# Performance work log

Measured on AMD Instinct MI355X. Metric: run time of the kernel, lower is better.

The kernel has to match this reference:

```python
import jax, jax.numpy as jnp
import numpy as np
import math

B, S, E, H, FF = 8, 1024, 1024, 16, 4096
HD = E // H
N_DOM = 1024          # boolean-domain size used in the custom scale
LN_EPS = 1e-5


def _layernorm(x, g, b, eps=LN_EPS):
    mu = jnp.mean(x, axis=-1, keepdims=True)
    var = jnp.var(x, axis=-1, keepdims=True)
    return (x - mu) * jax.lax.rsqrt(var + eps) * g + b


def setup_inputs() -> dict:
    key = jax.random.key(0)
    ks = jax.random.split(key, 8)
    s_e = 1.0 / math.sqrt(E)
    s_f = 1.0 / math.sqrt(FF)
    return {
        "x": jax.random.normal(ks[0], (B, S, E), jnp.float32),
        "in_proj_w": jax.random.normal(ks[1], (3 * E, E), jnp.float32) * s_e,
        "out_proj_w": jax.random.normal(ks[2], (E, E), jnp.float32) * s_e,
        "ln1_g": jnp.ones((E,), jnp.float32),
        "ln1_b": jnp.zeros((E,), jnp.float32),
        "ln2_g": jnp.ones((E,), jnp.float32),
        "ln2_b": jnp.zeros((E,), jnp.float32),
        "w1": jax.random.normal(ks[3], (FF, E), jnp.float32) * s_e,
        "b1": jax.random.normal(ks[4], (FF,), jnp.float32) * 0.01,
        "w2": jax.random.normal(ks[5], (E, FF), jnp.float32) * s_f,
        "b2": jax.random.normal(ks[6], (E,), jnp.float32) * 0.01,
    }


def reference(x, in_proj_w, out_proj_w, ln1_g, ln1_b, ln2_g, ln2_b, w1, b1, w2, b2):
    # --- custom multi-head attention (bias=False, dropout=0) ---
    qkv = jnp.einsum("bse,fe->bsf", x, in_proj_w)              # [B,S,3E]
    q, k, v = jnp.split(qkv, 3, axis=-1)
    q = q.reshape(B, S, H, HD)
    k = k.reshape(B, S, H, HD)
    v = v.reshape(B, S, H, HD)
    # nonstandard scale: sqrt(1/head_dim) * 2 * log(N)
    scale = math.sqrt(1.0 / HD) * 2.0 * math.log(N_DOM)
    scores = jnp.einsum("bqhd,bkhd->bhqk", q * scale, k)       # [B,H,S,S]
    attn = jax.nn.softmax(scores, axis=-1)
    ctx = jnp.einsum("bhqk,bkhd->bqhd", attn, v).reshape(B, S, E)
    attn_out = jnp.einsum("bse,fe->bsf", ctx, out_proj_w)      # [B,S,E]
    # --- residual + norm + FFN + residual + norm ---
    h = _layernorm(x + attn_out, ln1_g, ln1_b)
    ff = jnp.einsum("bsf,ef->bse", jax.nn.relu(jnp.einsum("bse,fe->bsf", h, w1) + b1), w2) + b2
    return _layernorm(h + ff, ln2_g, ln2_b)
```

## Files before the change

### kernel.cpp

```cpp
#include <hip/hip_runtime.h>
#include <cstdint>
#include <cmath>


typedef _Float16 f16;
typedef _Float16 f16x8 __attribute__((ext_vector_type(8)));
typedef _Float16 f16x4 __attribute__((ext_vector_type(4)));
typedef __bf16   bf16;
typedef __bf16   bf16x8 __attribute__((ext_vector_type(8)));
typedef __bf16   bf16x4 __attribute__((ext_vector_type(4)));
typedef __bf16   bf16x2 __attribute__((ext_vector_type(2)));
typedef float    f32x4  __attribute__((ext_vector_type(4)));
typedef float    f32x16 __attribute__((ext_vector_type(16)));
typedef unsigned int uint2v __attribute__((ext_vector_type(2)));
typedef unsigned int u32x4v __attribute__((ext_vector_type(4)));

#define B_SZ  8
#define S_SZ  1024
#define E_SZ  1024
#define H_SZ  16
#define HD_SZ 64
#define FF_SZ 4096
#define MTOK  (B_SZ * S_SZ)

__device__ __forceinline__ void async_ld16(const void* g, void* l) {
  __builtin_amdgcn_global_load_lds(
      (const __attribute__((address_space(1))) void*)(uintptr_t)g,
      (__attribute__((address_space(3))) void*)(uint32_t)(uintptr_t)l,
      16, 0, 0);
}

template <int N>
__device__ __forceinline__ void wait_vm() {
  if constexpr (N == 0)      asm volatile("s_waitcnt vmcnt(0)" ::: "memory");
  else if constexpr (N == 3) asm volatile("s_waitcnt vmcnt(3)" ::: "memory");
  else if constexpr (N == 4) asm volatile("s_waitcnt vmcnt(4)" ::: "memory");
  else static_assert(N == 0 || N == 3 || N == 4, "unsupported vmcnt");
  __builtin_amdgcn_sched_barrier(0);
}

__device__ __forceinline__ void wait_lgkm0_fenced() {
  asm volatile("s_waitcnt lgkmcnt(0)" ::: "memory");
  __builtin_amdgcn_sched_barrier(0);
}

__device__ __forceinline__ void permswap(uint32_t& a, uint32_t& b) {
  uint2v r = __builtin_amdgcn_permlane32_swap(a, b, false, false);
  a = r[0];
  b = r[1];
}

__global__ void cast_kernel(const float* __restrict__ in, f16* __restrict__ out, int n4) {
  int i = blockIdx.x * blockDim.x + threadIdx.x;
  if (i < n4) {
    float4 f = ((const float4*)in)[i];
    f16x4 o = {(f16)f.x, (f16)f.y, (f16)f.z, (f16)f.w};
    ((f16x4*)out)[i] = o;
  }
}

template <int BN, bool OUT_F16, bool RELU>
__global__ __launch_bounds__(512, 2)
void gemm256(const f16* __restrict__ A, const f16* __restrict__ Bm,
             const float* __restrict__ bias, void* __restrict__ Cp,
             int M, int N, int K, int bf16_from_col) {
  static_assert(BN == 256 || BN == 128, "BN must be 256 or 128");
  constexpr int NBCH  = (BN == 256) ? 2 : 1;
  constexpr int CHUNK = 4096;
  constexpr int NIF   = 2 + NBCH;
  constexpr int WN    = (BN == 256) ? 4 : 2;
  constexpr int FM    = (BN == 256) ? 8 : 4;

  __shared__ f16 lds[(8 + 4 * NBCH) * CHUNK];
  f16* Ab = lds;
  f16* Bb = lds + 8 * CHUNK;

  const int tid  = threadIdx.x;
  const int wave = tid >> 6;
  const int lane = tid & 63;
  const int quad = lane >> 4;
  const int l16  = lane & 15;

  const int wm  = wave / WN;
  const int wn  = wave % WN;
  const int ah  = (BN == 256) ? wm : (wm >> 1);
  const int amB = (BN == 256) ? 0 : (wm & 1) * 64;
  const int bh  = (BN == 256) ? (wn >> 1) : 0;
  const int bnB = (BN == 256) ? (wn & 1) * 64 : wn * 64;

  int logical = blockIdx.x;
  {
    const int nwg = gridDim.x;
    if ((nwg & 7) == 0) logical = (logical & 7) * (nwg >> 3) + (logical >> 3);
  }
  const int gx = N / BN;
  const int bn = logical % gx;
  const int bm = logical / gx;

  f32x4 acc[FM][4];
#pragma unroll
  for (int mi = 0; mi < FM; mi++)
#pragma unroll
    for (int ni = 0; ni < 4; ni++) acc[mi][ni] = (f32x4){0.f, 0.f, 0.f, 0.f};

  const int rr_s = tid >> 2;
  const int lo_s = (tid & 3) ^ ((rr_s >> 1) & 3);
  const int wofs = wave * 512;
  const f16* gAb = A  + ((size_t)bm * 256 + rr_s) * (size_t)K + lo_s * 8;
  const f16* gBb = Bm + ((size_t)bn * BN  + rr_s) * (size_t)K + lo_s * 8;

  auto stA = [&](int bb, int s, int h, int kt) {
    async_ld16(gAb + (size_t)h * 128 * K + kt * 64 + s * 32,
               Ab + ((((bb << 1) + s) << 1) + h) * CHUNK + wofs);
  };
  auto stB = [&](int bb, int s, int h, int kt) {
    async_ld16(gBb + (size_t)h * 128 * K + kt * 64 + s * 32,
               Bb + (((bb << 1) + s) * NBCH + h) * CHUNK + wofs);
  };
  auto rdFrag = [&](const f16* ch, int rr) -> f16x8 {
    return *(const f16x8*)&ch[rr * 32 + ((quad ^ ((rr >> 1) & 3)) << 3)];
  };

  const int NT = K >> 6;

#pragma unroll
  for (int s = 0; s < 2; s++) {
    stA(0, s, 0, 0);
    stA(0, s, 1, 0);
    stB(0, s, 0, 0);
    if constexpr (NBCH == 2) stB(0, s, 1, 0);
  }
  wait_vm<NIF>();
  __builtin_amdgcn_s_barrier();

  for (int t = 0; t < NT; t++) {
    const int cur = t & 1, oth = cur ^ 1;
    const bool last = (t == NT - 1);
#pragma unroll
    for (int s = 0; s < 2; s++) {
      const f16* Ach = Ab + ((((cur << 1) + s) << 1) + ah) * CHUNK;
      const f16* Bch = Bb + (((cur << 1) + s) * NBCH + bh) * CHUNK;

      f16x8 bfr[4], af[4];
#pragma unroll
      for (int ni = 0; ni < 4; ni++) bfr[ni] = rdFrag(Bch, bnB + ni * 16 + l16);
#pragma unroll
      for (int i = 0; i < 4; i++) af[i] = rdFrag(Ach, amB + i * 16 + l16);
      if (!last) {
        stA(oth, s, 0, t + 1);
        stA(oth, s, 1, t + 1);
        if constexpr (NBCH == 1) stB(oth, s, 0, t + 1);
      }
      __builtin_amdgcn_sched_barrier(0);
      __builtin_amdgcn_s_barrier();
      wait_lgkm0_fenced();
      __builtin_amdgcn_s_setprio(1);
#pragma unroll
      for (int i = 0; i < 4; i++)
#pragma unroll
        for (int ni = 0; ni < 4; ni++)
          acc[i][ni] = __builtin_amdgcn_mfma_f32_16x16x32_f16(af[i], bfr[ni], acc[i][ni], 0, 0, 0);
      __builtin_amdgcn_s_setprio(0);

      if constexpr (BN == 256) {
        __builtin_amdgcn_s_barrier();
#pragma unroll
        for (int i = 0; i < 4; i++) af[i] = rdFrag(Ach, amB + (4 + i) * 16 + l16);
        if (!last) {
          stB(oth, s, 0, t + 1);
          stB(oth, s, 1, t + 1);
        }
        __builtin_amdgcn_sched_barrier(0);
        __builtin_amdgcn_s_barrier();
        wait_lgkm0_fenced();
        __builtin_amdgcn_s_setprio(1);
#pragma unroll
        for (int i = 0; i < 4; i++)
#pragma unroll
          for (int ni = 0; ni < 4; ni++)
            acc[4 + i][ni] = __builtin_amdgcn_mfma_f32_16x16x32_f16(af[i], bfr[ni], acc[4 + i][ni], 0, 0, 0);
        __builtin_amdgcn_s_setprio(0);
      }

      if (!last) {
        wait_vm<NIF>();
        __builtin_amdgcn_s_barrier();
      } else if (s == 0) {
        wait_vm<0>();
        __builtin_amdgcn_s_barrier();
      }
    }
  }

  const int rowW = bm * 256 + ((BN == 256) ? wm * 128 : wm * 64);
  const int colW = bn * BN + wn * 64;
  const bool store_bf16 = OUT_F16 && (bn * BN >= bf16_from_col);
#pragma unroll
  for (int ni = 0; ni < 4; ni++) {
    const int col = colW + ni * 16 + l16;
    const float bv = (bias != nullptr) ? bias[col] : 0.f;
#pragma unroll
    for (int mi = 0; mi < FM; mi++) {
#pragma unroll
      for (int r = 0; r < 4; r++) {
        const int row = rowW + mi * 16 + quad * 4 + r;
        float v = acc[mi][ni][r] + bv;
        if (RELU) v = fmaxf(v, 0.f);
        if (OUT_F16) {
          if (store_bf16)
            ((bf16*)Cp)[(size_t)row * N + col] = (bf16)v;
          else
            ((f16*)Cp)[(size_t)row * N + col] = (f16)v;
        } else {
          ((float*)Cp)[(size_t)row * N + col] = v;
        }
      }
    }
  }
  (void)M;
}

__global__ __launch_bounds__(256, 4)
void attn_kernel(const f16* __restrict__ qkv, f16* __restrict__ ctx,
                 float scale2, float c2) {
  __shared__ __align__(16) char pool[33280];
  f16*  Ks = (f16*)pool;
  bf16* Vt = (bf16*)(pool + 16384);

  const int tid  = threadIdx.x;
  const int wave = tid >> 6;
  const int lane = tid & 63;
  const int l31  = lane & 31;
  const int hi   = lane >> 5;

  const int flat = blockIdx.x;
  const int bh   = flat & 127;
  const int qt   = flat >> 7;
  const int b    = bh >> 4;
  const int h    = bh & 15;

  const int rs = 3 * E_SZ;
  const size_t tokbase = (size_t)b * S_SZ;

  const int su  = lane >> 3;
  const int soc = (lane & 7) ^ su;

  {
    const f16* gq = qkv + (tokbase + qt * 128 + wave * 8 + su) * (size_t)rs + h * HD_SZ + soc * 8;
#pragma unroll
    for (int i = 0; i < 4; i++)
      async_ld16(gq + (size_t)i * 32 * rs, pool + (i * 32 + wave * 8) * 128);
  }
  __syncthreads();

  f16x8 aq[4];
  {
    const int qrow = wave * 32 + l31;
#pragma unroll
    for (int ks = 0; ks < 4; ks++)
      aq[ks] = *(const f16x8*)&Ks[qrow * 64 + (((ks * 2 + hi) ^ (qrow & 7)) << 3)];
  }

  float Lp = 0.f;
  f32x16 oacc[2];
#pragma unroll
  for (int nb = 0; nb < 2; nb++)
#pragma unroll
    for (int i = 0; i < 16; i++) oacc[nb][i] = 0.f;

  const int vc  = (tid & 7) * 8;
  const int vk0 = (tid >> 3) * 4;

  for (int t = 0; t < S_SZ / 128; t++) {
    __syncthreads();
    {
      const f16* gk = qkv + (tokbase + t * 128 + wave * 8 + su) * (size_t)rs + E_SZ + h * HD_SZ + soc * 8;
#pragma unroll
      for (int i = 0; i < 4; i++)
        async_ld16(gk + (size_t)i * 32 * rs, pool + (i * 32 + wave * 8) * 128);
    }
    {
      const bf16* gv = (const bf16*)qkv + (tokbase + t * 128 + vk0) * (size_t)rs + 2 * E_SZ + h * HD_SZ + vc;
      bf16x8 v0 = *(const bf16x8*)(gv);
      bf16x8 v1 = *(const bf16x8*)(gv + rs);
      bf16x8 v2 = *(const bf16x8*)(gv + 2 * rs);
      bf16x8 v3 = *(const bf16x8*)(gv + 3 * rs);
#pragma unroll
      for (int e = 0; e < 8; e++) {
        bf16x4 pk = {v0[e], v1[e], v2[e], v3[e]};
        *(bf16x4*)&Vt[(vc + e) * 132 + vk0] = pk;
      }
    }
    __syncthreads();

#pragma unroll
    for (int nt = 0; nt < 4; nt++) {
      f32x16 sacc;
#pragma unroll
      for (int i = 0; i < 16; i++) sacc[i] = 0.f;

      const int krow = nt * 32 + l31;
      __builtin_amdgcn_s_setprio(1);
#pragma unroll
      for (int ks = 0; ks < 4; ks++) {
        f16x8 kf = *(const f16x8*)&Ks[krow * 64 + (((ks * 2 + hi) ^ (krow & 7)) << 3)];
        sacc = __builtin_amdgcn_mfma_f32_32x32x16_f16(kf, aq[ks], sacc, 0, 0, 0);
      }
      __builtin_amdgcn_s_setprio(0);

      uint32_t w[8];
#pragma unroll
      for (int j = 0; j < 8; j++) {
        float p0 = exp2f(fmaf(sacc[2 * j],     scale2, -c2));
        float p1 = exp2f(fmaf(sacc[2 * j + 1], scale2, -c2));
        Lp += p0 + p1;
        bf16x2 pk2 = {(bf16)p0, (bf16)p1};
        w[j] = __builtin_bit_cast(uint32_t, pk2);
      }
      permswap(w[0], w[2]);
      permswap(w[1], w[3]);
      permswap(w[4], w[6]);
      permswap(w[5], w[7]);
      u32x4v pe = {w[0], w[1], w[2], w[3]};
      u32x4v po = {w[4], w[5], w[6], w[7]};
      bf16x8 pa[2] = {__builtin_bit_cast(bf16x8, pe), __builtin_bit_cast(bf16x8, po)};

      __builtin_amdgcn_s_setprio(1);
#pragma unroll
      for (int nb = 0; nb < 2; nb++) {
        const int d = nb * 32 + l31;
#pragma unroll
        for (int kst = 0; kst < 2; kst++) {
          const int key = (nt * 2 + kst) * 16 + hi * 8;
          bf16x4 blo = *(const bf16x4*)&Vt[d * 132 + key];
          bf16x4 bhi = *(const bf16x4*)&Vt[d * 132 + key + 4];
          bf16x8 bv = __builtin_shufflevector(blo, bhi, 0, 1, 2, 3, 4, 5, 6, 7);
          oacc[nb] = __builtin_amdgcn_mfma_f32_32x32x16_bf16(pa[kst], bv, oacc[nb], 0, 0, 0);
        }
      }
      __builtin_amdgcn_s_setprio(0);
    }
  }

  float Lfull = Lp + __shfl_xor(Lp, 32, 64);
  const float inv = 1.f / Lfull;
#pragma unroll
  for (int r = 0; r < 16; r++) {
    const int qrow = (r & 3) + 8 * (r >> 2) + 4 * hi;
    const float invr = __shfl(inv, qrow, 32);
    const size_t row = tokbase + (size_t)qt * 128 + wave * 32 + qrow;
#pragma unroll
    for (int nb = 0; nb < 2; nb++)
      ctx[row * (size_t)E_SZ + h * HD_SZ + nb * 32 + l31] = (f16)(oacc[nb][r] * invr);
  }
}

__global__ void ln_kernel(const float* __restrict__ a, const float* __restrict__ res,
                          const float* __restrict__ g, const float* __restrict__ bta,
                          float* __restrict__ out32, f16* __restrict__ out16) {
  const int row  = blockIdx.x;
  const int tid  = threadIdx.x;
  const int wave = tid >> 6;
  const int lane = tid & 63;
  const size_t base = (size_t)row * 1024;
  const int c = tid * 4;

  float4 va = *(const float4*)&a[base + c];
  float4 vr = *(const float4*)&res[base + c];
  float v0 = va.x + vr.x, v1 = va.y + vr.y, v2 = va.z + vr.z, v3 = va.w + vr.w;

  __shared__ float r1[4], r2[4];
  float s = v0 + v1 + v2 + v3;
#pragma unroll
  for (int off = 32; off; off >>= 1) s += __shfl_xor(s, off, 64);
  if (lane == 0) r1[wave] = s;
  __syncthreads();
  const float mu = (r1[0] + r1[1] + r1[2] + r1[3]) * (1.f / 1024.f);

  float d0 = v0 - mu, d1 = v1 - mu, d2 = v2 - mu, d3 = v3 - mu;
  float ss = d0 * d0 + d1 * d1 + d2 * d2 + d3 * d3;
#pragma unroll
  for (int off = 32; off; off >>= 1) ss += __shfl_xor(ss, off, 64);
  if (lane == 0) r2[wave] = ss;
  __syncthreads();
  const float var = (r2[0] + r2[1] + r2[2] + r2[3]) * (1.f / 1024.f);
  const float rsq = rsqrtf(var + 1e-5f);

  float4 gg = *(const float4*)&g[c];
  float4 bb = *(const float4*)&bta[c];
  float o0 = d0 * rsq * gg.x + bb.x;
  float o1 = d1 * rsq * gg.y + bb.y;
  float o2 = d2 * rsq * gg.z + bb.z;
  float o3 = d3 * rsq * gg.w + bb.w;
  float4 o = {o0, o1, o2, o3};
  *(float4*)&out32[base + c] = o;
  if (out16 != nullptr) {
    f16x4 ob = {(f16)o0, (f16)o1, (f16)o2, (f16)o3};
    *(f16x4*)&out16[base + c] = ob;
  }
}

extern "C" void kernel_launch(void* const* d_in, const int* in_sizes, int n_in,
                              void* d_out, int out_size, void* d_ws, size_t ws_size,
                              hipStream_t stream) {
  const float* x    = (const float*)d_in[0];
  const float* wqkv = (const float*)d_in[1];
  const float* wo   = (const float*)d_in[2];
  const float* ln1g = (const float*)d_in[3];
  const float* ln1b = (const float*)d_in[4];
  const float* ln2g = (const float*)d_in[5];
  const float* ln2b = (const float*)d_in[6];
  const float* w1   = (const float*)d_in[7];
  const float* b1   = (const float*)d_in[8];
  const float* w2   = (const float*)d_in[9];
  const float* b2   = (const float*)d_in[10];
  float* out = (float*)d_out;

  char* ws = (char*)d_ws;
  f16* w_inb  = (f16*)(ws + 0);
  f16* w_outb = (f16*)(ws + 6291456);
  f16* w1b    = (f16*)(ws + 8388608);
  f16* w2b    = (f16*)(ws + 16777216);
  f16* xb     = (f16*)(ws + 25165824);
  f16* qkv    = (f16*)(ws + 41943040);
  f16* ctx    = (f16*)(ws + 92274688);
  f16* ff1    = (f16*)(ws + 41943040);
  float* tmp  = (float*)(ws + 109051904);
  float* hbuf = (float*)(ws + 142606336);
  f16* hb     = xb;

  const int NOBF = 1 << 30;

  cast_kernel<<<3072, 256, 0, stream>>>(wqkv, w_inb, 3 * E_SZ * E_SZ / 4);
  cast_kernel<<<1024, 256, 0, stream>>>(wo, w_outb, E_SZ * E_SZ / 4);
  cast_kernel<<<4096, 256, 0, stream>>>(w1, w1b, FF_SZ * E_SZ / 4);
  cast_kernel<<<4096, 256, 0, stream>>>(w2, w2b, E_SZ * FF_SZ / 4);
  cast_kernel<<<8192, 256, 0, stream>>>(x, xb, MTOK * E_SZ / 4);

  gemm256<256, true, false><<<(3 * E_SZ / 256) * (MTOK / 256), 512, 0, stream>>>(
      xb, w_inb, nullptr, qkv, MTOK, 3 * E_SZ, E_SZ, 2048);

  attn_kernel<<<1024, 256, 0, stream>>>(qkv, ctx, 2.5f, 60.0f);

  gemm256<128, false, false><<<(E_SZ / 128) * (MTOK / 256), 512, 0, stream>>>(
      ctx, w_outb, nullptr, tmp, MTOK, E_SZ, E_SZ, NOBF);

  ln_kernel<<<MTOK, 256, 0, stream>>>(tmp, x, ln1g, ln1b, hbuf, hb);

  gemm256<256, true, true><<<(FF_SZ / 256) * (MTOK / 256), 512, 0, stream>>>(
      hb, w1b, b1, ff1, MTOK, FF_SZ, E_SZ, NOBF);

  gemm256<128, false, false><<<(E_SZ / 128) * (MTOK / 256), 512, 0, stream>>>(
      ff1, w2b, b2, tmp, MTOK, E_SZ, FF_SZ, NOBF);

  ln_kernel<<<MTOK, 256, 0, stream>>>(tmp, hbuf, ln2g, ln2b, out, nullptr);

  (void)in_sizes; (void)n_in; (void)out_size; (void)ws_size;
}
```

Before: 494.7 us.

## Transpose MFMA operands, stage f16 epilogue through LDS, remap tiles per XCD

Swaps the MFMA operand order so each lane holds four consecutive output columns. This lets the fp32 epilogue use 16-byte vector stores and bias loads. The f16/bf16 epilogue now writes through a swizzled LDS tile and then does fully coalesced 16-byte row stores, replacing scattered 2-byte global stores. It also adds an XCD-aware block remapping that groups 2x4 tile clusters per XCD for better L2 reuse, at the cost of an extra LDS round trip and two barriers in the epilogue.

Measured after the change: 492.4 us. No clear change (-0.5%).

```diff
diff --git a/kernel.cpp b/kernel.cpp
--- a/kernel.cpp
+++ b/kernel.cpp
@@ -65,6 +65,7 @@
              const float* __restrict__ bias, void* __restrict__ Cp,
              int M, int N, int K, int bf16_from_col) {
   static_assert(BN == 256 || BN == 128, "BN must be 256 or 128");
+  static_assert(!(OUT_F16 && BN == 128), "f16 LDS epilogue requires BN==256");
   constexpr int NBCH  = (BN == 256) ? 2 : 1;
   constexpr int CHUNK = 4096;
   constexpr int NIF   = 2 + NBCH;
@@ -88,14 +89,27 @@
   const int bh  = (BN == 256) ? (wn >> 1) : 0;
   const int bnB = (BN == 256) ? (wn & 1) * 64 : wn * 64;
 
-  int logical = blockIdx.x;
+  const int gx = N / BN;
+  int bm, bn;
   {
+    const int b   = blockIdx.x;
     const int nwg = gridDim.x;
-    if ((nwg & 7) == 0) logical = (logical & 7) * (nwg >> 3) + (logical >> 3);
-  }
-  const int gx = N / BN;
-  const int bn = logical % gx;
-  const int bm = logical / gx;
+    const int gm  = nwg / gx;
+    if (((nwg & 63) == 0) && ((gx & 1) == 0) && ((gm & 3) == 0)) {
+      const int xcd = b & 7;
+      const int seq = b >> 3;
+      const int st  = xcd + ((seq >> 3) << 3);
+      const int pos = seq & 7;
+      const int nstx = gx >> 1;
+      bn = (st % nstx) * 2 + (pos & 1);
+      bm = (st / nstx) * 4 + (pos >> 1);
+    } else {
+      int logical = b;
+      if ((nwg & 7) == 0) logical = (logical & 7) * (nwg >> 3) + (logical >> 3);
+      bn = logical % gx;
+      bm = logical / gx;
+    }
+  }
 
   f32x4 acc[FM][4];
 #pragma unroll
@@ -159,7 +173,7 @@
       for (int i = 0; i < 4; i++)
 #pragma unroll
         for (int ni = 0; ni < 4; ni++)
-          acc[i][ni] = __builtin_amdgcn_mfma_f32_16x16x32_f16(af[i], bfr[ni], acc[i][ni], 0, 0, 0);
+          acc[i][ni] = __builtin_amdgcn_mfma_f32_16x16x32_f16(bfr[ni], af[i], acc[i][ni], 0, 0, 0);
       __builtin_amdgcn_s_setprio(0);
 
       if constexpr (BN == 256) {
@@ -178,7 +192,7 @@
         for (int i = 0; i < 4; i++)
 #pragma unroll
           for (int ni = 0; ni < 4; ni++)
-            acc[4 + i][ni] = __builtin_amdgcn_mfma_f32_16x16x32_f16(af[i], bfr[ni], acc[4 + i][ni], 0, 0, 0);
+            acc[4 + i][ni] = __builtin_amdgcn_mfma_f32_16x16x32_f16(bfr[ni], af[i], acc[4 + i][ni], 0, 0, 0);
         __builtin_amdgcn_s_setprio(0);
       }
 
@@ -192,28 +206,80 @@
     }
   }
 
-  const int rowW = bm * 256 + ((BN == 256) ? wm * 128 : wm * 64);
-  const int colW = bn * BN + wn * 64;
-  const bool store_bf16 = OUT_F16 && (bn * BN >= bf16_from_col);
-#pragma unroll
-  for (int ni = 0; ni < 4; ni++) {
-    const int col = colW + ni * 16 + l16;
-    const float bv = (bias != nullptr) ? bias[col] : 0.f;
-#pragma unroll
-    for (int mi = 0; mi < FM; mi++) {
-#pragma unroll
-      for (int r = 0; r < 4; r++) {
-        const int row = rowW + mi * 16 + quad * 4 + r;
-        float v = acc[mi][ni][r] + bv;
-        if (RELU) v = fmaxf(v, 0.f);
-        if (OUT_F16) {
-          if (store_bf16)
-            ((bf16*)Cp)[(size_t)row * N + col] = (bf16)v;
-          else
-            ((f16*)Cp)[(size_t)row * N + col] = (f16)v;
-        } else {
-          ((float*)Cp)[(size_t)row * N + col] = v;
+  if constexpr (!OUT_F16) {
+    const int rowG0 = bm * 256 + ((BN == 256) ? wm * 128 : wm * 64);
+    const int colG0 = bn * BN + wn * 64;
+    float* Cf = (float*)Cp;
+#pragma unroll
+    for (int ni = 0; ni < 4; ni++) {
+      const int col = colG0 + ni * 16 + quad * 4;
+      float4 bv = {0.f, 0.f, 0.f, 0.f};
+      if (bias != nullptr) bv = *(const float4*)&bias[col];
+#pragma unroll
+      for (int mi = 0; mi < FM; mi++) {
+        const int row = rowG0 + mi * 16 + l16;
+        float v0 = acc[mi][ni][0] + bv.x;
+        float v1 = acc[mi][ni][1] + bv.y;
+        float v2 = acc[mi][ni][2] + bv.z;
+        float v3 = acc[mi][ni][3] + bv.w;
+        if (RELU) {
+          v0 = fmaxf(v0, 0.f); v1 = fmaxf(v1, 0.f);
+          v2 = fmaxf(v2, 0.f); v3 = fmaxf(v3, 0.f);
         }
+        f32x4 o = {v0, v1, v2, v3};
+        *(f32x4*)&Cf[(size_t)row * N + col] = o;
+      }
+    }
+  } else {
+    __syncthreads();
+    {
+      char* cb = (char*)lds;
+      const int rowL0 = wm * 128;
+      const int colL0 = wn * 64;
+      const bool store_bf16 = (bn * BN >= bf16_from_col);
+#pragma unroll
+      for (int mi = 0; mi < FM; mi++) {
+        const int row = rowL0 + mi * 16 + l16;
+        const int sw  = row & 7;
+#pragma unroll
+        for (int ni = 0; ni < 4; ni++) {
+          const int col = colL0 + ni * 16 + quad * 4;
+          float4 bv = {0.f, 0.f, 0.f, 0.f};
+          if (bias != nullptr) bv = *(const float4*)&bias[bn * BN + col];
+          float v0 = acc[mi][ni][0] + bv.x;
+          float v1 = acc[mi][ni][1] + bv.y;
+          float v2 = acc[mi][ni][2] + bv.z;
+          float v3 = acc[mi][ni][3] + bv.w;
+          if (RELU) {
+            v0 = fmaxf(v0, 0.f); v1 = fmaxf(v1, 0.f);
+            v2 = fmaxf(v2, 0.f); v3 = fmaxf(v3, 0.f);
+          }
+          const int ch = (col >> 3) ^ sw;
+          char* p = cb + row * 512 + (ch << 4) + ((quad & 1) << 3);
+          if (store_bf16) {
+            bf16x4 o = {(bf16)v0, (bf16)v1, (bf16)v2, (bf16)v3};
+            *(bf16x4*)p = o;
+          } else {
+            f16x4 o = {(f16)v0, (f16)v1, (f16)v2, (f16)v3};
+            *(f16x4*)p = o;
+          }
+        }
+      }
+    }
+    __syncthreads();
+    {
+      const char* cb = (const char*)lds;
+      const int rr0 = tid >> 5;
+      const int cc  = tid & 31;
+      const size_t rowBytes = (size_t)N * 2;
+      char* gbase = (char*)Cp + (size_t)(bm * 256) * rowBytes
+                  + (size_t)bn * BN * 2 + (size_t)cc * 16;
+#pragma unroll
+      for (int it = 0; it < 16; it++) {
+        const int row = it * 16 + rr0;
+        const int ch  = cc ^ (row & 7);
+        u32x4v v = *(const u32x4v*)(cb + row * 512 + (ch << 4));
+        *(u32x4v*)(gbase + (size_t)row * rowBytes) = v;
       }
     }
   }
```
